# Kernel tuning notes

Hardware: AMD Instinct MI355X
Metric: run time of the kernel (lower is better)

Reference implementation:

```python
import jax, jax.numpy as jnp
import numpy as np

DIM = 96
EPS = 1e-5

def setup_inputs() -> dict:
    key = jax.random.key(0)
    k1, k2, k3, k4 = jax.random.split(key, 4)
    x = jax.random.normal(k1, (2, DIM, 32, 64, 64), dtype=jnp.float32)
    # LayerNorm(8*dim) params and Linear(8*dim -> 2*dim, bias=False) weight
    gamma = jnp.ones((8 * DIM,), dtype=jnp.float32)
    beta = jnp.zeros((8 * DIM,), dtype=jnp.float32)
    w_red = jax.random.normal(k2, (8 * DIM, 2 * DIM), dtype=jnp.float32) * (1.0 / np.sqrt(8 * DIM))
    return {"x": x, "gamma": gamma, "beta": beta, "w_red": w_red}


def _patch_merge(x, gamma, beta, w_red):
    B, C, D, H, W = x.shape
    # pad trailing spatial dims to even (static shapes -> python ifs are fine)
    if (D % 2) or (H % 2) or (W % 2):
        x = jnp.pad(x, ((0, 0), (0, 0), (0, D % 2), (0, H % 2), (0, W % 2)))
    x = jnp.transpose(x, (0, 2, 3, 4, 1))  # B, D, H, W, C
    # gather the 8 octant sub-lattices and concat on channel
    parts = [x[:, d::2, h::2, w::2, :]
             for d in (0, 1) for h in (0, 1) for w in (0, 1)]
    # torch order: x0..x7 indexed by (d,h,w) bits with d slowest -> matches loop order
    y = jnp.concatenate(parts, axis=-1)  # B, D/2, H/2, W/2, 8C
    # LayerNorm over last dim
    mu = jnp.mean(y, axis=-1, keepdims=True)
    var = jnp.mean(jnp.square(y - mu), axis=-1, keepdims=True)
    y = (y - mu) * jax.lax.rsqrt(var + EPS) * gamma + beta
    # Linear 8C -> 2C, no bias
    y = jnp.einsum('bdhwc,co->bdhwo', y, w_red)
    return jnp.transpose(y, (0, 4, 1, 2, 3))  # B, 2C, D/2, H/2, W/2


def reference(x, gamma, beta, w_red):
    return _patch_merge(x, gamma, beta, w_red)
```

## Files before the change

### kernel.cpp

```cpp
#include <hip/hip_runtime.h>

typedef __attribute__((ext_vector_type(8))) short short8;
typedef __attribute__((ext_vector_type(4))) float float4v;

__device__ __forceinline__ unsigned short f2bf(float f) {
  unsigned int u = __float_as_uint(f);
  u += 0x7fffu + ((u >> 16) & 1u);
  return (unsigned short)(u >> 16);
}
__device__ __forceinline__ float bf2f(unsigned short h) {
  return __uint_as_float(((unsigned int)h) << 16);
}

__global__ __launch_bounds__(256)
void prep_kernel(const float* __restrict__ w_red, const float* __restrict__ gamma,
                 const float* __restrict__ beta, unsigned short* __restrict__ w_bf,
                 float* __restrict__ colsum, float* __restrict__ bias) {
  const int n = blockIdx.x;
  const int t = threadIdx.x;
  float cs = 0.f, bs = 0.f;
#pragma unroll
  for (int j = 0; j < 3; ++j) {
    int kp = j * 256 + t;
    int ko = (kp & 7) * 96 + (kp >> 3);
    float w = w_red[(size_t)ko * 192 + n];
    unsigned short v = f2bf(gamma[ko] * w);
    w_bf[(size_t)n * 768 + kp] = v;
    cs += bf2f(v);
    bs += beta[ko] * w;
  }
#pragma unroll
  for (int off = 1; off < 64; off <<= 1) {
    cs += __shfl_xor(cs, off, 64);
    bs += __shfl_xor(bs, off, 64);
  }
  __shared__ float red[2][4];
  const int wave = t >> 6;
  if ((t & 63) == 0) { red[0][wave] = cs; red[1][wave] = bs; }
  __syncthreads();
  if (t == 0) {
    colsum[n] = red[0][0] + red[0][1] + red[0][2] + red[0][3];
    bias[n]   = red[1][0] + red[1][1] + red[1][2] + red[1][3];
  }
}

__global__ __launch_bounds__(256, 3)
void pm_kernel(const float* __restrict__ x, const unsigned short* __restrict__ w_bf,
               const float* __restrict__ colsum, const float* __restrict__ bias,
               float* __restrict__ out) {
  __shared__ __align__(16) unsigned short Y[32][776];
  __shared__ float4 part4[4][16];
  __shared__ float smu[32], srs[32];

  const int tid = threadIdx.x;
  const int bid = blockIdx.x;
  const int b  = bid >> 9;
  const int dz = (bid >> 5) & 15;
  const int hy = bid & 31;

  const float* xb = x + (size_t)b * 12582912u + (size_t)dz * 8192u + (size_t)hy * 128u;

  const int r0 = tid >> 4;
  const int c0 = r0 >> 2;
  const int di = (r0 >> 1) & 1;
  const int hi = r0 & 1;
  const int w0 = (tid & 15) << 2;
  const float* xp = xb + (size_t)c0 * 131072u + di * 4096 + hi * 64 + w0;

  float4 v[24];
#pragma unroll
  for (int it = 0; it < 24; ++it)
    v[it] = *(const float4*)(xp + (size_t)it * 524288u);

  const int lane = tid & 63;
  const int wave = tid >> 6;
  const int lrow = lane & 15;
  const int lq   = lane >> 4;
  const unsigned short* wrow[3];
#pragma unroll
  for (int t3 = 0; t3 < 3; ++t3)
    wrow[t3] = w_bf + (size_t)((wave * 3 + t3) * 16 + lrow) * 768 + lq * 8;
  short8 b0[3], b1[3];
#pragma unroll
  for (int t3 = 0; t3 < 3; ++t3) b0[t3] = *(const short8*)(wrow[t3]);
#pragma unroll
  for (int t3 = 0; t3 < 3; ++t3) b1[t3] = *(const short8*)(wrow[t3] + 32);

  const int wx0 = (tid & 15) << 1;
  const int k00 = c0 * 8 + di * 4 + hi * 2;
  float sum0 = 0.f, sq0 = 0.f, sum1 = 0.f, sq1 = 0.f;
#pragma unroll
  for (int it = 0; it < 24; ++it) {
    float4 vv = v[it];
    unsigned int p01 = (unsigned int)f2bf(vv.x) | ((unsigned int)f2bf(vv.y) << 16);
    unsigned int p23 = (unsigned int)f2bf(vv.z) | ((unsigned int)f2bf(vv.w) << 16);
    int k0 = it * 32 + k00;
    *(unsigned int*)&Y[wx0][k0]     = p01;
    *(unsigned int*)&Y[wx0 + 1][k0] = p23;
    sum0 += vv.x + vv.y;  sq0 += vv.x * vv.x + vv.y * vv.y;
    sum1 += vv.z + vv.w;  sq1 += vv.z * vv.z + vv.w * vv.w;
  }
#pragma unroll
  for (int off = 16; off < 64; off <<= 1) {
    sum0 += __shfl_xor(sum0, off, 64);  sq0 += __shfl_xor(sq0, off, 64);
    sum1 += __shfl_xor(sum1, off, 64);  sq1 += __shfl_xor(sq1, off, 64);
  }
  if (lane < 16) part4[wave][lane] = make_float4(sum0, sq0, sum1, sq1);
  __syncthreads();

  if (tid < 32) {
    int sp = tid >> 1, odd = tid & 1;
    float s = 0.f, q = 0.f;
#pragma unroll
    for (int w = 0; w < 4; ++w) {
      float4 p = part4[w][sp];
      s += odd ? p.z : p.x;
      q += odd ? p.w : p.y;
    }
    float mu  = s * (1.f / 768.f);
    float var = q * (1.f / 768.f) - mu * mu;
    smu[tid] = mu;
    srs[tid] = rsqrtf(var + 1e-5f);
  }

  float4v acc[2][3];
#pragma unroll
  for (int i2 = 0; i2 < 2; ++i2)
#pragma unroll
    for (int j2 = 0; j2 < 3; ++j2)
#pragma unroll
      for (int r = 0; r < 4; ++r) acc[i2][j2][r] = 0.f;

  for (int kc = 0; kc < 24; ++kc) {
    int kn = (kc + 2 <= 23) ? kc + 2 : 23;
    short8 b2[3];
#pragma unroll
    for (int t3 = 0; t3 < 3; ++t3) b2[t3] = *(const short8*)(wrow[t3] + kn * 32);
    short8 a0 = *(const short8*)&Y[lrow][kc * 32 + lq * 8];
    short8 a1 = *(const short8*)&Y[16 + lrow][kc * 32 + lq * 8];
#pragma unroll
    for (int t3 = 0; t3 < 3; ++t3) {
      acc[0][t3] = __builtin_amdgcn_mfma_f32_16x16x32_bf16(a0, b0[t3], acc[0][t3], 0, 0, 0);
      acc[1][t3] = __builtin_amdgcn_mfma_f32_16x16x32_bf16(a1, b0[t3], acc[1][t3], 0, 0, 0);
    }
#pragma unroll
    for (int t3 = 0; t3 < 3; ++t3) { b0[t3] = b1[t3]; b1[t3] = b2[t3]; }
  }

  float cs_n[3], bi_n[3];
#pragma unroll
  for (int t3 = 0; t3 < 3; ++t3) {
    int ng = (wave * 3 + t3) * 16 + lrow;
    cs_n[t3] = colsum[ng];
    bi_n[t3] = bias[ng];
  }

  __syncthreads();
  float* Cs = (float*)&Y[0][0];
#pragma unroll
  for (int t3 = 0; t3 < 3; ++t3) {
    int ng = (wave * 3 + t3) * 16 + lrow;
#pragma unroll
    for (int mt = 0; mt < 2; ++mt)
#pragma unroll
      for (int r = 0; r < 4; ++r) {
        int m = mt * 16 + lq * 4 + r;
        float vv = srs[m] * (acc[mt][t3][r] - smu[m] * cs_n[t3]) + bi_n[t3];
        Cs[ng * 40 + m] = vv;
      }
  }
  __syncthreads();

  float* ob = out + (size_t)b * 3145728u + (size_t)dz * 1024u + (size_t)hy * 32u;
#pragma unroll
  for (int it = 0; it < 6; ++it) {
    int idx4 = it * 256 + tid;
    int o  = idx4 >> 3;
    int wq = idx4 & 7;
    float4 vv = *(const float4*)&Cs[o * 40 + wq * 4];
    *(float4*)(ob + (size_t)o * 16384u + wq * 4) = vv;
  }
}

extern "C" void kernel_launch(void* const* d_in, const int* in_sizes, int n_in,
                              void* d_out, int out_size, void* d_ws, size_t ws_size,
                              hipStream_t stream) {
  const float* x     = (const float*)d_in[0];
  const float* gamma = (const float*)d_in[1];
  const float* beta  = (const float*)d_in[2];
  const float* w_red = (const float*)d_in[3];
  float* out = (float*)d_out;

  unsigned short* w_bf = (unsigned short*)d_ws;
  float* colsum = (float*)((char*)d_ws + 294912);
  float* bias   = colsum + 192;

  prep_kernel<<<dim3(192), dim3(256), 0, stream>>>(w_red, gamma, beta, w_bf, colsum, bias);
  pm_kernel<<<dim3(1024), dim3(256), 0, stream>>>(x, w_bf, colsum, bias, out);
}
```

Baseline: 189.3 us.

## Halve tokens per block, double grid, write MFMA results directly to global

Each block now handles 16 output tokens (half a W row) instead of 32, so the grid doubles to 2048 blocks and per-thread register and LDS use drop, allowing a launch bound of 6 blocks per CU. The LDS staging of the output tile and its extra barrier are removed; each lane writes its float4 of normalized accumulators straight to global memory. The weight-fragment loads are moved after the LDS fill. In exchange, global loads and stores use shorter contiguous runs (128B rows and 64B output segments), and weight fragments are reloaded by twice as many blocks.

```diff
diff --git a/kernel.cpp b/kernel.cpp
--- a/kernel.cpp
+++ b/kernel.cpp
@@ -44,38 +44,62 @@
   }
 }
 
-__global__ __launch_bounds__(256, 3)
+__global__ __launch_bounds__(256, 6)
 void pm_kernel(const float* __restrict__ x, const unsigned short* __restrict__ w_bf,
                const float* __restrict__ colsum, const float* __restrict__ bias,
                float* __restrict__ out) {
-  __shared__ __align__(16) unsigned short Y[32][776];
-  __shared__ float4 part4[4][16];
-  __shared__ float smu[32], srs[32];
+  __shared__ __align__(16) unsigned short Y[16][776];
+  __shared__ float4 part4[4][8];
+  __shared__ float smu[16], srs[16];
 
   const int tid = threadIdx.x;
   const int bid = blockIdx.x;
-  const int b  = bid >> 9;
-  const int dz = (bid >> 5) & 15;
-  const int hy = bid & 31;
+  const int b  = bid >> 10;
+  const int dz = (bid >> 6) & 15;
+  const int hy = (bid >> 1) & 31;
+  const int wh = bid & 1;
 
-  const float* xb = x + (size_t)b * 12582912u + (size_t)dz * 8192u + (size_t)hy * 128u;
+  const float* xb = x + (size_t)b * 12582912u + (size_t)dz * 8192u
+                      + (size_t)hy * 128u + wh * 32;
 
-  const int r0 = tid >> 4;
+  const int r0 = tid >> 3;
   const int c0 = r0 >> 2;
   const int di = (r0 >> 1) & 1;
   const int hi = r0 & 1;
-  const int w0 = (tid & 15) << 2;
+  const int w0 = (tid & 7) << 2;
   const float* xp = xb + (size_t)c0 * 131072u + di * 4096 + hi * 64 + w0;
 
-  float4 v[24];
+  float4 v[12];
 #pragma unroll
-  for (int it = 0; it < 24; ++it)
-    v[it] = *(const float4*)(xp + (size_t)it * 524288u);
+  for (int it = 0; it < 12; ++it)
+    v[it] = *(const float4*)(xp + (size_t)it * 1048576u);
 
   const int lane = tid & 63;
   const int wave = tid >> 6;
   const int lrow = lane & 15;
   const int lq   = lane >> 4;
+
+  const int wx0 = (tid & 7) << 1;
+  const int k00 = c0 * 8 + di * 4 + hi * 2;
+  float sum0 = 0.f, sq0 = 0.f, sum1 = 0.f, sq1 = 0.f;
+#pragma unroll
+  for (int it = 0; it < 12; ++it) {
+    float4 vv = v[it];
+    unsigned int p01 = (unsigned int)f2bf(vv.x) | ((unsigned int)f2bf(vv.y) << 16);
+    unsigned int p23 = (unsigned int)f2bf(vv.z) | ((unsigned int)f2bf(vv.w) << 16);
+    int k0 = it * 64 + k00;
+    *(unsigned int*)&Y[wx0][k0]     = p01;
+    *(unsigned int*)&Y[wx0 + 1][k0] = p23;
+    sum0 += vv.x + vv.y;  sq0 += vv.x * vv.x + vv.y * vv.y;
+    sum1 += vv.z + vv.w;  sq1 += vv.z * vv.z + vv.w * vv.w;
+  }
+#pragma unroll
+  for (int off = 8; off < 64; off <<= 1) {
+    sum0 += __shfl_xor(sum0, off, 64);  sq0 += __shfl_xor(sq0, off, 64);
+    sum1 += __shfl_xor(sum1, off, 64);  sq1 += __shfl_xor(sq1, off, 64);
+  }
+  if (lane < 8) part4[wave][lane] = make_float4(sum0, sq0, sum1, sq1);
+
   const unsigned short* wrow[3];
 #pragma unroll
   for (int t3 = 0; t3 < 3; ++t3)
@@ -86,34 +110,14 @@
 #pragma unroll
   for (int t3 = 0; t3 < 3; ++t3) b1[t3] = *(const short8*)(wrow[t3] + 32);
 
-  const int wx0 = (tid & 15) << 1;
-  const int k00 = c0 * 8 + di * 4 + hi * 2;
-  float sum0 = 0.f, sq0 = 0.f, sum1 = 0.f, sq1 = 0.f;
-#pragma unroll
-  for (int it = 0; it < 24; ++it) {
-    float4 vv = v[it];
-    unsigned int p01 = (unsigned int)f2bf(vv.x) | ((unsigned int)f2bf(vv.y) << 16);
-    unsigned int p23 = (unsigned int)f2bf(vv.z) | ((unsigned int)f2bf(vv.w) << 16);
-    int k0 = it * 32 + k00;
-    *(unsigned int*)&Y[wx0][k0]     = p01;
-    *(unsigned int*)&Y[wx0 + 1][k0] = p23;
-    sum0 += vv.x + vv.y;  sq0 += vv.x * vv.x + vv.y * vv.y;
-    sum1 += vv.z + vv.w;  sq1 += vv.z * vv.z + vv.w * vv.w;
-  }
-#pragma unroll
-  for (int off = 16; off < 64; off <<= 1) {
-    sum0 += __shfl_xor(sum0, off, 64);  sq0 += __shfl_xor(sq0, off, 64);
-    sum1 += __shfl_xor(sum1, off, 64);  sq1 += __shfl_xor(sq1, off, 64);
-  }
-  if (lane < 16) part4[wave][lane] = make_float4(sum0, sq0, sum1, sq1);
   __syncthreads();
 
-  if (tid < 32) {
-    int sp = tid >> 1, odd = tid & 1;
+  if (tid < 16) {
+    int l = tid >> 1, odd = tid & 1;
     float s = 0.f, q = 0.f;
 #pragma unroll
     for (int w = 0; w < 4; ++w) {
-      float4 p = part4[w][sp];
+      float4 p = part4[w][l];
       s += odd ? p.z : p.x;
       q += odd ? p.w : p.y;
     }
@@ -121,30 +125,6 @@
     float var = q * (1.f / 768.f) - mu * mu;
     smu[tid] = mu;
     srs[tid] = rsqrtf(var + 1e-5f);
-  }
-
-  float4v acc[2][3];
-#pragma unroll
-  for (int i2 = 0; i2 < 2; ++i2)
-#pragma unroll
-    for (int j2 = 0; j2 < 3; ++j2)
-#pragma unroll
-      for (int r = 0; r < 4; ++r) acc[i2][j2][r] = 0.f;
-
-  for (int kc = 0; kc < 24; ++kc) {
-    int kn = (kc + 2 <= 23) ? kc + 2 : 23;
-    short8 b2[3];
-#pragma unroll
-    for (int t3 = 0; t3 < 3; ++t3) b2[t3] = *(const short8*)(wrow[t3] + kn * 32);
-    short8 a0 = *(const short8*)&Y[lrow][kc * 32 + lq * 8];
-    short8 a1 = *(const short8*)&Y[16 + lrow][kc * 32 + lq * 8];
-#pragma unroll
-    for (int t3 = 0; t3 < 3; ++t3) {
-      acc[0][t3] = __builtin_amdgcn_mfma_f32_16x16x32_bf16(a0, b0[t3], acc[0][t3], 0, 0, 0);
-      acc[1][t3] = __builtin_amdgcn_mfma_f32_16x16x32_bf16(a1, b0[t3], acc[1][t3], 0, 0, 0);
-    }
-#pragma unroll
-    for (int t3 = 0; t3 < 3; ++t3) { b0[t3] = b1[t3]; b1[t3] = b2[t3]; }
   }
 
   float cs_n[3], bi_n[3];
@@ -156,29 +136,39 @@
   }
 
   __syncthreads();
-  float* Cs = (float*)&Y[0][0];
+
+  float4v acc[3];
+#pragma unroll
+  for (int j2 = 0; j2 < 3; ++j2)
+#pragma unroll
+    for (int r = 0; r < 4; ++r) acc[j2][r] = 0.f;
+
+  for (int kc = 0; kc < 24; ++kc) {
+    int kn = (kc + 2 <= 23) ? kc + 2 : 23;
+    short8 b2[3];
+#pragma unroll
+    for (int t3 = 0; t3 < 3; ++t3) b2[t3] = *(const short8*)(wrow[t3] + kn * 32);
+    short8 a0 = *(const short8*)&Y[lrow][kc * 32 + lq * 8];
+#pragma unroll
+    for (int t3 = 0; t3 < 3; ++t3)
+      acc[t3] = __builtin_amdgcn_mfma_f32_16x16x32_bf16(a0, b0[t3], acc[t3], 0, 0, 0);
+#pragma unroll
+    for (int t3 = 0; t3 < 3; ++t3) { b0[t3] = b1[t3]; b1[t3] = b2[t3]; }
+  }
+
+  float4 mu4 = *(const float4*)&smu[lq * 4];
+  float4 rs4 = *(const float4*)&srs[lq * 4];
+  float* ob = out + (size_t)b * 3145728u + (size_t)dz * 1024u
+                  + (size_t)hy * 32u + wh * 16 + lq * 4;
 #pragma unroll
   for (int t3 = 0; t3 < 3; ++t3) {
     int ng = (wave * 3 + t3) * 16 + lrow;
-#pragma unroll
-    for (int mt = 0; mt < 2; ++mt)
-#pragma unroll
-      for (int r = 0; r < 4; ++r) {
-        int m = mt * 16 + lq * 4 + r;
-        float vv = srs[m] * (acc[mt][t3][r] - smu[m] * cs_n[t3]) + bi_n[t3];
-        Cs[ng * 40 + m] = vv;
-      }
-  }
-  __syncthreads();
-
-  float* ob = out + (size_t)b * 3145728u + (size_t)dz * 1024u + (size_t)hy * 32u;
-#pragma unroll
-  for (int it = 0; it < 6; ++it) {
-    int idx4 = it * 256 + tid;
-    int o  = idx4 >> 3;
-    int wq = idx4 & 7;
-    float4 vv = *(const float4*)&Cs[o * 40 + wq * 4];
-    *(float4*)(ob + (size_t)o * 16384u + wq * 4) = vv;
+    float4 vv;
+    vv.x = rs4.x * (acc[t3][0] - mu4.x * cs_n[t3]) + bi_n[t3];
+    vv.y = rs4.y * (acc[t3][1] - mu4.y * cs_n[t3]) + bi_n[t3];
+    vv.z = rs4.z * (acc[t3][2] - mu4.z * cs_n[t3]) + bi_n[t3];
+    vv.w = rs4.w * (acc[t3][3] - mu4.w * cs_n[t3]) + bi_n[t3];
+    *(float4*)(ob + (size_t)ng * 16384u) = vv;
   }
 }
 
@@ -196,5 +186,5 @@
   float* bias   = colsum + 192;
 
   prep_kernel<<<dim3(192), dim3(256), 0, stream>>>(w_red, gamma, beta, w_bf, colsum, bias);
-  pm_kernel<<<dim3(1024), dim3(256), 0, stream>>>(x, w_bf, colsum, bias, out);
+  pm_kernel<<<dim3(2048), dim3(256), 0, stream>>>(x, w_bf, colsum, bias, out);
 }
```

Result: slower. 219.4 us (+15.9%).

## Split patch-merge into gather/LayerNorm-stats kernel and separate MFMA GEMM kernel

Applied to the files above, without the earlier changes.

Unfuses the single patch-merge kernel into two stages. A gather kernel loads x through global_load_lds, packs the values to bf16, computes per-token mean and rstd, and writes the bf16 token matrix to workspace. A GEMM kernel then multiplies it by the weights with MFMA, each wave producing 16 rows by all 192 outputs. This is meant to raise occupancy and reuse of the weight tiles, at the cost of a 48MB round trip through global memory and an extra launch. The old fused kernel is kept as a fallback for when the workspace is too small.

```diff
diff --git a/kernel.cpp b/kernel.cpp
--- a/kernel.cpp
+++ b/kernel.cpp
@@ -10,6 +10,9 @@
 }
 __device__ __forceinline__ float bf2f(unsigned short h) {
   return __uint_as_float(((unsigned int)h) << 16);
+}
+__device__ __forceinline__ unsigned int pack2bf(float a, float b) {
+  return (unsigned int)f2bf(a) | ((unsigned int)f2bf(b) << 16);
 }
 
 __global__ __launch_bounds__(256)
@@ -45,9 +48,166 @@
 }
 
 __global__ __launch_bounds__(256, 3)
-void pm_kernel(const float* __restrict__ x, const unsigned short* __restrict__ w_bf,
-               const float* __restrict__ colsum, const float* __restrict__ bias,
-               float* __restrict__ out) {
+void gather_kernel(const float* __restrict__ x, unsigned short* __restrict__ Yg,
+                   float* __restrict__ mu_g, float* __restrict__ rs_g) {
+  __shared__ __align__(16) float Yf[12288];
+  __shared__ float4 part4[4][8];
+
+  const int tid = threadIdx.x;
+  const int bid = blockIdx.x;
+  const int b  = bid >> 10;
+  const int dz = (bid >> 6) & 15;
+  const int hy = (bid >> 1) & 31;
+  const int wh = bid & 1;
+
+  const float* xb = x + (size_t)b * 12582912u + (size_t)dz * 8192u
+                      + (size_t)hy * 128u + wh * 32;
+
+  const int r0 = tid >> 3;
+  const int c0 = r0 >> 2;
+  const int di = (r0 >> 1) & 1;
+  const int hi = r0 & 1;
+  const int w0 = (tid & 7) << 2;
+  const float* xp = xb + (size_t)c0 * 131072u + di * 4096 + hi * 64 + w0;
+
+  const int lane = tid & 63;
+  const int wave = tid >> 6;
+
+  {
+    const float* ldsbase = &Yf[wave * 3072];
+#pragma unroll
+    for (int it = 0; it < 12; ++it) {
+      __builtin_amdgcn_global_load_lds(
+          (const __attribute__((address_space(1))) unsigned int*)(xp + (size_t)it * 1048576u),
+          (__attribute__((address_space(3))) unsigned int*)(ldsbase + it * 256),
+          16, 0, 0);
+    }
+  }
+  __syncthreads();
+
+  unsigned int pr0[12], pr1[12];
+  float sum0 = 0.f, sq0 = 0.f, sum1 = 0.f, sq1 = 0.f;
+#pragma unroll
+  for (int it = 0; it < 12; ++it) {
+    float4 vv = *(const float4*)&Yf[(wave * 12 + it) * 256 + lane * 4];
+    pr0[it] = pack2bf(vv.x, vv.y);
+    pr1[it] = pack2bf(vv.z, vv.w);
+    sum0 += vv.x + vv.y;  sq0 += vv.x * vv.x + vv.y * vv.y;
+    sum1 += vv.z + vv.w;  sq1 += vv.z * vv.z + vv.w * vv.w;
+  }
+#pragma unroll
+  for (int off = 8; off < 64; off <<= 1) {
+    sum0 += __shfl_xor(sum0, off, 64);  sq0 += __shfl_xor(sq0, off, 64);
+    sum1 += __shfl_xor(sum1, off, 64);  sq1 += __shfl_xor(sq1, off, 64);
+  }
+  if (lane < 8) part4[wave][lane] = make_float4(sum0, sq0, sum1, sq1);
+
+  __syncthreads();
+
+  unsigned short (*Y)[776] = (unsigned short (*)[776])Yf;
+  const int wx0 = (tid & 7) << 1;
+  const int k00 = c0 * 8 + di * 4 + hi * 2;
+#pragma unroll
+  for (int it = 0; it < 12; ++it) {
+    int k0 = it * 64 + k00;
+    *(unsigned int*)&Y[wx0][k0]     = pr0[it];
+    *(unsigned int*)&Y[wx0 + 1][k0] = pr1[it];
+  }
+
+  if (tid < 16) {
+    int l = tid >> 1, odd = tid & 1;
+    float s = 0.f, q = 0.f;
+#pragma unroll
+    for (int w = 0; w < 4; ++w) {
+      float4 p = part4[w][l];
+      s += odd ? p.z : p.x;
+      q += odd ? p.w : p.y;
+    }
+    float mu  = s * (1.f / 768.f);
+    float var = q * (1.f / 768.f) - mu * mu;
+    mu_g[bid * 16 + tid] = mu;
+    rs_g[bid * 16 + tid] = rsqrtf(var + 1e-5f);
+  }
+
+  __syncthreads();
+
+  unsigned short* yrow = Yg + (size_t)bid * 12288u;
+#pragma unroll
+  for (int it = 0; it < 6; ++it) {
+    int o   = it * 256 + tid;
+    int row = o / 96;
+    int col = o - row * 96;
+    float4 vv = *(const float4*)&Y[row][col * 8];
+    *(float4*)(yrow + row * 768 + col * 8) = vv;
+  }
+}
+
+__global__ __launch_bounds__(256, 2)
+void gemm_kernel(const unsigned short* __restrict__ Yg,
+                 const unsigned short* __restrict__ w_bf,
+                 const float* __restrict__ mu_g, const float* __restrict__ rs_g,
+                 const float* __restrict__ colsum, const float* __restrict__ bias,
+                 float* __restrict__ out) {
+  const int tid  = threadIdx.x;
+  const int lane = tid & 63;
+  const int wave = tid >> 6;
+  const int lrow = lane & 15;
+  const int lq   = lane >> 4;
+  const int m0   = blockIdx.x * 64 + wave * 16;
+
+  const unsigned short* arow = Yg + (size_t)(m0 + lrow) * 768 + lq * 8;
+  const unsigned short* brow = w_bf + (size_t)lrow * 768 + lq * 8;
+
+  float4v acc[12];
+#pragma unroll
+  for (int j = 0; j < 12; ++j)
+#pragma unroll
+    for (int r = 0; r < 4; ++r) acc[j][r] = 0.f;
+
+  short8 a_cur = *(const short8*)(arow);
+  short8 b_cur[12];
+#pragma unroll
+  for (int j = 0; j < 12; ++j) b_cur[j] = *(const short8*)(brow + (size_t)j * 12288u);
+
+  for (int kc = 0; kc < 24; ++kc) {
+    int kn = (kc + 1 < 24) ? kc + 1 : 23;
+    short8 a_nxt = *(const short8*)(arow + kn * 32);
+    short8 b_nxt[12];
+#pragma unroll
+    for (int j = 0; j < 12; ++j)
+      b_nxt[j] = *(const short8*)(brow + (size_t)j * 12288u + kn * 32);
+#pragma unroll
+    for (int j = 0; j < 12; ++j)
+      acc[j] = __builtin_amdgcn_mfma_f32_16x16x32_bf16(a_cur, b_cur[j], acc[j], 0, 0, 0);
+    a_cur = a_nxt;
+#pragma unroll
+    for (int j = 0; j < 12; ++j) b_cur[j] = b_nxt[j];
+  }
+
+  float4 mu4 = *(const float4*)&mu_g[m0 + lq * 4];
+  float4 rs4 = *(const float4*)&rs_g[m0 + lq * 4];
+  const int bb   = m0 >> 14;
+  const int rem  = m0 & 16383;
+  const int dz   = rem >> 10;
+  const int rem2 = rem & 1023;
+  float* ob = out + (size_t)bb * 3145728u + (size_t)dz * 1024u + rem2 + lq * 4;
+#pragma unroll
+  for (int j = 0; j < 12; ++j) {
+    int n = j * 16 + lrow;
+    float cs = colsum[n], bi = bias[n];
+    float4 vv;
+    vv.x = rs4.x * (acc[j][0] - mu4.x * cs) + bi;
+    vv.y = rs4.y * (acc[j][1] - mu4.y * cs) + bi;
+    vv.z = rs4.z * (acc[j][2] - mu4.z * cs) + bi;
+    vv.w = rs4.w * (acc[j][3] - mu4.w * cs) + bi;
+    *(float4*)(ob + (size_t)n * 16384u) = vv;
+  }
+}
+
+__global__ __launch_bounds__(256, 3)
+void pm_fallback(const float* __restrict__ x, const unsigned short* __restrict__ w_bf,
+                 const float* __restrict__ colsum, const float* __restrict__ bias,
+                 float* __restrict__ out) {
   __shared__ __align__(16) unsigned short Y[32][776];
   __shared__ float4 part4[4][16];
   __shared__ float smu[32], srs[32];
@@ -59,7 +219,6 @@
   const int hy = bid & 31;
 
   const float* xb = x + (size_t)b * 12582912u + (size_t)dz * 8192u + (size_t)hy * 128u;
-
   const int r0 = tid >> 4;
   const int c0 = r0 >> 2;
   const int di = (r0 >> 1) & 1;
@@ -92,8 +251,8 @@
 #pragma unroll
   for (int it = 0; it < 24; ++it) {
     float4 vv = v[it];
-    unsigned int p01 = (unsigned int)f2bf(vv.x) | ((unsigned int)f2bf(vv.y) << 16);
-    unsigned int p23 = (unsigned int)f2bf(vv.z) | ((unsigned int)f2bf(vv.w) << 16);
+    unsigned int p01 = pack2bf(vv.x, vv.y);
+    unsigned int p23 = pack2bf(vv.z, vv.w);
     int k0 = it * 32 + k00;
     *(unsigned int*)&Y[wx0][k0]     = p01;
     *(unsigned int*)&Y[wx0 + 1][k0] = p23;
@@ -191,10 +350,25 @@
   const float* w_red = (const float*)d_in[3];
   float* out = (float*)d_out;
 
-  unsigned short* w_bf = (unsigned short*)d_ws;
-  float* colsum = (float*)((char*)d_ws + 294912);
-  float* bias   = colsum + 192;
-
-  prep_kernel<<<dim3(192), dim3(256), 0, stream>>>(w_red, gamma, beta, w_bf, colsum, bias);
-  pm_kernel<<<dim3(1024), dim3(256), 0, stream>>>(x, w_bf, colsum, bias, out);
-}
+  const size_t Y_BYTES = 50331648u;
+  const size_t NEED = Y_BYTES + 294912u + 768u + 768u + 131072u + 131072u;
+
+  if (ws_size >= NEED) {
+    unsigned short* Yg   = (unsigned short*)d_ws;
+    unsigned short* w_bf = (unsigned short*)((char*)d_ws + Y_BYTES);
+    float* colsum = (float*)((char*)d_ws + Y_BYTES + 294912u);
+    float* bias   = colsum + 192;
+    float* mu_g   = (float*)((char*)d_ws + Y_BYTES + 294912u + 1536u);
+    float* rs_g   = mu_g + 32768;
+
+    prep_kernel<<<dim3(192), dim3(256), 0, stream>>>(w_red, gamma, beta, w_bf, colsum, bias);
+    gather_kernel<<<dim3(2048), dim3(256), 0, stream>>>(x, Yg, mu_g, rs_g);
+    gemm_kernel<<<dim3(512), dim3(256), 0, stream>>>(Yg, w_bf, mu_g, rs_g, colsum, bias, out);
+  } else {
+    unsigned short* w_bf = (unsigned short*)d_ws;
+    float* colsum = (float*)((char*)d_ws + 294912u);
+    float* bias   = colsum + 192;
+    prep_kernel<<<dim3(192), dim3(256), 0, stream>>>(w_red, gamma, beta, w_bf, colsum, bias);
+    pm_fallback<<<dim3(1024), dim3(256), 0, stream>>>(x, w_bf, colsum, bias, out);
+  }
+}
```

Measured after the change: 244.9 us. 1.29x slower.
